# Performance work log

Measured on AMD Instinct MI355X. Metric: run time of the kernel, lower is better.

Reference implementation:

```python
import jax, jax.numpy as jnp
import numpy as np

DIM = 1024
HEADS = 16
HEAD_DIM = DIM // HEADS
SCALE = HEAD_DIM ** -0.5


def setup_inputs() -> dict:
    key = jax.random.key(0)
    k_x, k_win, k_wout, k_bout = jax.random.split(key, 4)
    x = jax.random.normal(k_x, (4, 2048, DIM), dtype=jnp.float32)
    # torch Linear: y = x @ W.T + b; store weights as [in, out] for jnp
    w_in = jax.random.normal(k_win, (DIM, 3 * DIM), dtype=jnp.float32) * (DIM ** -0.5)
    w_out = jax.random.normal(k_wout, (DIM, DIM), dtype=jnp.float32) * (DIM ** -0.5)
    b_out = jax.random.normal(k_bout, (DIM,), dtype=jnp.float32) * 0.02
    return {"x": x, "w_in": w_in, "w_out": w_out, "b_out": b_out}


def reference(x, w_in, w_out, b_out):
    b, n, _ = x.shape
    qkv = x @ w_in  # [b, n, 3*dim]
    q, k, v = jnp.split(qkv, 3, axis=-1)
    # [b, n, h*d] -> [b, h, n, d]
    def split_heads(t):
        return t.reshape(b, n, HEADS, HEAD_DIM).transpose(0, 2, 1, 3)
    q, k, v = split_heads(q), split_heads(k), split_heads(v)
    scores = jnp.einsum('bhid,bhjd->bhij', q, k) * SCALE
    attn = jax.nn.softmax(scores, axis=-1)  # dropout_rate=0 -> identity
    o = jnp.einsum('bhij,bhjd->bhid', attn, v)
    o = o.transpose(0, 2, 1, 3).reshape(b, n, HEADS * HEAD_DIM)
    return o @ w_out + b_out
```

## Files before the change

### kernel.cpp

```cpp
#include <hip/hip_runtime.h>

typedef unsigned short u16;
typedef __bf16 bf16x8 __attribute__((ext_vector_type(8)));
typedef float f32x4 __attribute__((ext_vector_type(4)));
typedef unsigned short u16x4 __attribute__((ext_vector_type(4)));
typedef unsigned short u16x8 __attribute__((ext_vector_type(8)));

#define DIM 1024
#define HEADS 16
#define HD 64
#define SEQ 2048
#define BATCH 4
#define NROWS (BATCH*SEQ)
#define ATT_SCALE 0.125f

__device__ __forceinline__ u16 f2bf(float f) {
  union { float f; unsigned u; } v; v.f = f;
  unsigned r = v.u + 0x7FFFu + ((v.u >> 16) & 1u);
  return (u16)(r >> 16);
}

__device__ __forceinline__ f32x4 mfma16(bf16x8 a, bf16x8 b, f32x4 c) {
  return __builtin_amdgcn_mfma_f32_16x16x32_bf16(a, b, c, 0, 0, 0);
}

__device__ __forceinline__ void gl_lds16(const void* g, void* l) {
  __builtin_amdgcn_global_load_lds(
      (const __attribute__((address_space(1))) void*)g,
      (__attribute__((address_space(3))) void*)l, 16, 0, 0);
}

__global__ __launch_bounds__(256) void cast_f32_bf16(const float* __restrict__ in,
                                                     u16* __restrict__ out) {
  int i = blockIdx.x * 256 + threadIdx.x;
  float4 v = ((const float4*)in)[i];
  u16x4 o = { f2bf(v.x), f2bf(v.y), f2bf(v.z), f2bf(v.w) };
  *(u16x4*)(out + (size_t)i * 4) = o;
}

__global__ __launch_bounds__(256) void transpose_cast(const float* __restrict__ in,
                                                      u16* __restrict__ out,
                                                      int R, int C) {
  __shared__ u16 tile[64][65];
  int c0 = blockIdx.x * 64, r0 = blockIdx.y * 64;
  int tid = threadIdx.x;
#pragma unroll
  for (int i = 0; i < 16; ++i) {
    int idx = tid + i * 256;
    int r = idx >> 6, c = idx & 63;
    tile[c][r] = f2bf(in[(size_t)(r0 + r) * C + c0 + c]);
  }
  __syncthreads();
#pragma unroll
  for (int i = 0; i < 16; ++i) {
    int idx = tid + i * 256;
    int r = idx >> 6, c = idx & 63;
    out[(size_t)(c0 + r) * R + r0 + c] = tile[r][c];
  }
}

__global__ __launch_bounds__(256) void transpose_v(const u16* __restrict__ qkv,
                                                   u16* __restrict__ vT) {
  __shared__ unsigned t32[64][37];
  const int t = blockIdx.x, bh = blockIdx.y;
  const int b = bh >> 4, h = bh & 15;
  const u16* src = qkv + ((size_t)(b * SEQ + t * 64)) * 3072 + 2048 + h * 64;
  const int tid = threadIdx.x;
#pragma unroll
  for (int i = 0; i < 8; ++i) {
    int lin = tid + i * 256;
    int r2 = lin >> 6, c = lin & 63;
    unsigned lo = src[(size_t)(2 * r2) * 3072 + c];
    unsigned hi = src[(size_t)(2 * r2 + 1) * 3072 + c];
    t32[c][r2] = lo | (hi << 16);
  }
  __syncthreads();
  unsigned* dst = (unsigned*)(vT + (size_t)bh * 64 * 2048);
#pragma unroll
  for (int i = 0; i < 8; ++i) {
    int lin = tid + i * 256;
    int d = lin >> 5, r2 = lin & 31;
    dst[(size_t)d * 1024 + t * 32 + r2] = t32[d][r2];
  }
}

template<int OUT_F32>
__global__ __launch_bounds__(256) void gemm_bt(const u16* __restrict__ A,
                                               const u16* __restrict__ BT,
                                               void* __restrict__ Cout,
                                               const float* __restrict__ bias,
                                               int M, int N, int K) {
  __shared__ __align__(16) u16 As[128 * 64];
  __shared__ __align__(16) u16 Bs[128 * 64];
  const int tid = threadIdx.x;
  const int l = tid & 63, w = tid >> 6, g = l >> 4, ln = l & 15;
  const int m0 = blockIdx.y * 128, n0 = blockIdx.x * 128;
  const int wr = w >> 1, wc = w & 1;
  f32x4 acc[4][4];
#pragma unroll
  for (int i = 0; i < 4; ++i)
#pragma unroll
    for (int j = 0; j < 4; ++j) acc[i][j] = (f32x4){0.f, 0.f, 0.f, 0.f};

  const int srow = tid >> 3;
  const int scol = (tid & 7) * 8;
  const u16* Asrc = A  + (size_t)(m0 + srow) * K + scol;
  const u16* Bsrc = BT + (size_t)(n0 + srow) * K + scol;
  char* AsB = (char*)As + (size_t)w * 1024;
  char* BsB = (char*)Bs + (size_t)w * 1024;

  const int nk = K >> 6;
  for (int kt = 0; kt < nk; ++kt) {
    const u16* a0 = Asrc + kt * 64;
    const u16* b0 = Bsrc + kt * 64;
#pragma unroll
    for (int is = 0; is < 4; ++is) {
      gl_lds16(a0 + (size_t)is * 32 * K, AsB + is * 4096);
      gl_lds16(b0 + (size_t)is * 32 * K, BsB + is * 4096);
    }
    __syncthreads();
#pragma unroll
    for (int kk = 0; kk < 2; ++kk) {
      bf16x8 af[4], bfr[4];
#pragma unroll
      for (int i = 0; i < 4; ++i) {
        af[i]  = *(const bf16x8*)(As + (wr * 64 + i * 16 + ln) * 64 + kk * 32 + g * 8);
        bfr[i] = *(const bf16x8*)(Bs + (wc * 64 + i * 16 + ln) * 64 + kk * 32 + g * 8);
      }
#pragma unroll
      for (int mi = 0; mi < 4; ++mi)
#pragma unroll
        for (int ni = 0; ni < 4; ++ni)
          acc[mi][ni] = mfma16(af[mi], bfr[ni], acc[mi][ni]);
    }
    __syncthreads();
  }
#pragma unroll
  for (int mi = 0; mi < 4; ++mi) {
#pragma unroll
    for (int ni = 0; ni < 4; ++ni) {
      int col = n0 + wc * 64 + ni * 16 + ln;
#pragma unroll
      for (int j = 0; j < 4; ++j) {
        int row = m0 + wr * 64 + mi * 16 + g * 4 + j;
        float v = acc[mi][ni][j];
        if (OUT_F32) {
          ((float*)Cout)[(size_t)row * N + col] = v + bias[col];
        } else {
          ((u16*)Cout)[(size_t)row * N + col] = f2bf(v);
        }
      }
    }
  }
}

__global__ __launch_bounds__(256) void attn_kernel(const u16* __restrict__ qkv,
                                                   const u16* __restrict__ vT,
                                                   u16* __restrict__ obuf) {
  __shared__ __align__(16) u16 k_lds[64 * 64];
  __shared__ __align__(16) u16 v_lds[64 * 64];
  const int qt = blockIdx.x, h = blockIdx.y, b = blockIdx.z;
  const int tid = threadIdx.x;
  const int w = tid >> 6, l = tid & 63, g = l >> 4, ln = l & 15;
  const int qrow = qt * 64 + w * 16 + ln;
  const size_t rs = 3 * DIM;
  const u16* qb = qkv + (size_t)(b * SEQ + qrow) * rs + h * HD;
  bf16x8 qf0 = *(const bf16x8*)(qb + g * 8);
  bf16x8 qf1 = *(const bf16x8*)(qb + 32 + g * 8);

  const int krow = tid >> 3;
  const int ksrccol = ((((tid & 7) << 4) ^ ((krow & 7) << 4))) >> 1;
  const u16* kbase = qkv + (size_t)b * SEQ * rs + DIM + h * HD;
  const u16* vtb = vT + (size_t)(b * HEADS + h) * 64 * 2048;
  char* kdst = (char*)k_lds + (size_t)w * 1024;
  char* vdst = (char*)v_lds + (size_t)w * 1024;

  const int swz = (ln & 7) << 4;

  float m = -1e30f, lsum = 0.f;
  f32x4 of[4];
#pragma unroll
  for (int i = 0; i < 4; ++i) of[i] = (f32x4){0.f, 0.f, 0.f, 0.f};

  for (int kv0 = 0; kv0 < SEQ; kv0 += 64) {
    const u16* ks0 = kbase + (size_t)(kv0 + krow) * rs + ksrccol;
    const u16* vs0 = vtb + (size_t)krow * 2048 + kv0 + ksrccol;
    gl_lds16(ks0, kdst);
    gl_lds16(ks0 + (size_t)32 * rs, kdst + 4096);
    gl_lds16(vs0, vdst);
    gl_lds16(vs0 + (size_t)32 * 2048, vdst + 4096);
    __syncthreads();

    f32x4 sacc[4];
#pragma unroll
    for (int f = 0; f < 4; ++f) sacc[f] = (f32x4){0.f, 0.f, 0.f, 0.f};
#pragma unroll
    for (int f = 0; f < 4; ++f) {
      const char* kr = (const char*)k_lds + (f * 16 + ln) * 128;
      bf16x8 a0 = *(const bf16x8*)(kr + ((g * 16) ^ swz));
      bf16x8 a1 = *(const bf16x8*)(kr + ((64 | (g * 16)) ^ swz));
      sacc[f] = mfma16(a0, qf0, sacc[f]);
      sacc[f] = mfma16(a1, qf1, sacc[f]);
    }

    float tm = -1e30f;
#pragma unroll
    for (int f = 0; f < 4; ++f)
#pragma unroll
      for (int j = 0; j < 4; ++j) {
        float s = sacc[f][j] * ATT_SCALE;
        sacc[f][j] = s;
        tm = fmaxf(tm, s);
      }
    tm = fmaxf(tm, __shfl_xor(tm, 16));
    tm = fmaxf(tm, __shfl_xor(tm, 32));
    float mn = fmaxf(m, tm);
    float resc = __expf(m - mn);
    float ps = 0.f;
    union pu { u16x8 u; bf16x8 b; } pf[2];
#pragma unroll
    for (int f = 0; f < 4; ++f)
#pragma unroll
      for (int j = 0; j < 4; ++j) {
        float p = __expf(sacc[f][j] - mn);
        ps += p;
        pf[f >> 1].u[(f & 1) * 4 + j] = f2bf(p);
      }
    ps += __shfl_xor(ps, 16);
    ps += __shfl_xor(ps, 32);
    lsum = lsum * resc + ps;
    m = mn;
#pragma unroll
    for (int fd = 0; fd < 4; ++fd) of[fd] *= resc;

#pragma unroll
    for (int kk = 0; kk < 2; ++kk) {
#pragma unroll
      for (int fd = 0; fd < 4; ++fd) {
        const char* vr = (const char*)v_lds + (fd * 16 + ln) * 128;
        u16x4 lo = *(const u16x4*)(vr + ((64 * kk + 8 * g) ^ swz));
        u16x4 hi = *(const u16x4*)(vr + ((64 * kk + 32 + 8 * g) ^ swz));
        union { u16x8 u; bf16x8 b; } fa;
        fa.u = (u16x8){ lo[0], lo[1], lo[2], lo[3], hi[0], hi[1], hi[2], hi[3] };
        of[fd] = mfma16(fa.b, pf[kk].b, of[fd]);
      }
    }
    __syncthreads();
  }

  float linv = 1.f / lsum;
  u16* orow = obuf + (size_t)(b * SEQ + qrow) * DIM + h * HD;
#pragma unroll
  for (int fd = 0; fd < 4; ++fd) {
    u16x4 ov = { f2bf(of[fd][0] * linv), f2bf(of[fd][1] * linv),
                 f2bf(of[fd][2] * linv), f2bf(of[fd][3] * linv) };
    *(u16x4*)(orow + fd * 16 + g * 4) = ov;
  }
}

extern "C" void kernel_launch(void* const* d_in, const int* in_sizes, int n_in,
                              void* d_out, int out_size, void* d_ws, size_t ws_size,
                              hipStream_t stream) {
  const float* x     = (const float*)d_in[0];
  const float* w_in  = (const float*)d_in[1];
  const float* w_out = (const float*)d_in[2];
  const float* b_out = (const float*)d_in[3];
  float* out = (float*)d_out;

  char* ws = (char*)d_ws;
  u16* xb     = (u16*)(ws);
  u16* vT     = (u16*)(ws);
  u16* w_inT  = (u16*)(ws + (size_t)16 * 1024 * 1024);
  u16* w_outT = (u16*)(ws + (size_t)22 * 1024 * 1024);
  u16* qkv    = (u16*)(ws + (size_t)24 * 1024 * 1024);
  u16* obuf   = (u16*)(ws + (size_t)72 * 1024 * 1024);

  cast_f32_bf16<<<8192, 256, 0, stream>>>(x, xb);
  transpose_cast<<<dim3(48, 16), 256, 0, stream>>>(w_in, w_inT, 1024, 3072);
  transpose_cast<<<dim3(16, 16), 256, 0, stream>>>(w_out, w_outT, 1024, 1024);
  gemm_bt<0><<<dim3(24, 64), 256, 0, stream>>>(xb, w_inT, qkv, nullptr, NROWS, 3 * DIM, DIM);
  transpose_v<<<dim3(32, 64), 256, 0, stream>>>(qkv, vT);
  attn_kernel<<<dim3(32, HEADS, BATCH), 256, 0, stream>>>(qkv, vT, obuf);
  gemm_bt<1><<<dim3(8, 64), 256, 0, stream>>>(obuf, w_outT, out, b_out, NROWS, DIM, DIM);
}
```

Before: 277.3 us.

## Streamline attention softmax with exp2, deferred rescale, packed bf16 converts, XCD-aware grid

New measurement: 255.3 us. 1.09x faster.

```diff
diff --git a/kernel.cpp b/kernel.cpp
--- a/kernel.cpp
+++ b/kernel.cpp
@@ -12,12 +12,19 @@
 #define SEQ 2048
 #define BATCH 4
 #define NROWS (BATCH*SEQ)
-#define ATT_SCALE 0.125f
+#define C2 0.18033688f
+#define DEFER_THR 30.0f
 
 __device__ __forceinline__ u16 f2bf(float f) {
   union { float f; unsigned u; } v; v.f = f;
   unsigned r = v.u + 0x7FFFu + ((v.u >> 16) & 1u);
   return (u16)(r >> 16);
+}
+
+__device__ __forceinline__ unsigned cvt_pk_bf16(float lo, float hi) {
+  unsigned r;
+  asm("v_cvt_pk_bf16_f32 %0, %1, %2" : "=v"(r) : "v"(lo), "v"(hi));
+  return r;
 }
 
 __device__ __forceinline__ f32x4 mfma16(bf16x8 a, bf16x8 b, f32x4 c) {
@@ -159,7 +166,9 @@
                                                    u16* __restrict__ obuf) {
   __shared__ __align__(16) u16 k_lds[64 * 64];
   __shared__ __align__(16) u16 v_lds[64 * 64];
-  const int qt = blockIdx.x, h = blockIdx.y, b = blockIdx.z;
+  const int wg = blockIdx.x;
+  const int j = (wg & 7) * 256 + (wg >> 3);
+  const int qt = j & 31, h = (j >> 5) & 15, b = j >> 9;
   const int tid = threadIdx.x;
   const int w = tid >> 6, l = tid & 63, g = l >> 4, ln = l & 15;
   const int qrow = qt * 64 + w * 16 + ln;
@@ -203,45 +212,46 @@
       sacc[f] = mfma16(a1, qf1, sacc[f]);
     }
 
-    float tm = -1e30f;
+    float tm = -3e38f;
 #pragma unroll
     for (int f = 0; f < 4; ++f)
 #pragma unroll
-      for (int j = 0; j < 4; ++j) {
-        float s = sacc[f][j] * ATT_SCALE;
-        sacc[f][j] = s;
-        tm = fmaxf(tm, s);
-      }
+      for (int jj = 0; jj < 4; ++jj) tm = fmaxf(tm, sacc[f][jj]);
     tm = fmaxf(tm, __shfl_xor(tm, 16));
     tm = fmaxf(tm, __shfl_xor(tm, 32));
-    float mn = fmaxf(m, tm);
-    float resc = __expf(m - mn);
+    if (__any(tm > m + DEFER_THR)) {
+      float mn = fmaxf(m, tm);
+      float rs2 = __builtin_amdgcn_exp2f((m - mn) * C2);
+      lsum *= rs2;
+#pragma unroll
+      for (int fd = 0; fd < 4; ++fd) of[fd] *= rs2;
+      m = mn;
+    }
+    const float mc = m * C2;
     float ps = 0.f;
-    union pu { u16x8 u; bf16x8 b; } pf[2];
-#pragma unroll
-    for (int f = 0; f < 4; ++f)
-#pragma unroll
-      for (int j = 0; j < 4; ++j) {
-        float p = __expf(sacc[f][j] - mn);
-        ps += p;
-        pf[f >> 1].u[(f & 1) * 4 + j] = f2bf(p);
-      }
+    union pu { unsigned wd[4]; bf16x8 b; } pf[2];
+#pragma unroll
+    for (int f = 0; f < 4; ++f) {
+#pragma unroll
+      for (int j2 = 0; j2 < 2; ++j2) {
+        float p0 = __builtin_amdgcn_exp2f(fmaf(sacc[f][2 * j2], C2, -mc));
+        float p1 = __builtin_amdgcn_exp2f(fmaf(sacc[f][2 * j2 + 1], C2, -mc));
+        ps += p0 + p1;
+        pf[f >> 1].wd[(f & 1) * 2 + j2] = cvt_pk_bf16(p0, p1);
+      }
+    }
     ps += __shfl_xor(ps, 16);
     ps += __shfl_xor(ps, 32);
-    lsum = lsum * resc + ps;
-    m = mn;
-#pragma unroll
-    for (int fd = 0; fd < 4; ++fd) of[fd] *= resc;
+    lsum += ps;
 
 #pragma unroll
     for (int kk = 0; kk < 2; ++kk) {
 #pragma unroll
       for (int fd = 0; fd < 4; ++fd) {
         const char* vr = (const char*)v_lds + (fd * 16 + ln) * 128;
-        u16x4 lo = *(const u16x4*)(vr + ((64 * kk + 8 * g) ^ swz));
-        u16x4 hi = *(const u16x4*)(vr + ((64 * kk + 32 + 8 * g) ^ swz));
-        union { u16x8 u; bf16x8 b; } fa;
-        fa.u = (u16x8){ lo[0], lo[1], lo[2], lo[3], hi[0], hi[1], hi[2], hi[3] };
+        union { bf16x8 b; struct { u16x4 lo, hi; } hv; } fa;
+        fa.hv.lo = *(const u16x4*)(vr + ((64 * kk + 8 * g) ^ swz));
+        fa.hv.hi = *(const u16x4*)(vr + ((64 * kk + 32 + 8 * g) ^ swz));
         of[fd] = mfma16(fa.b, pf[kk].b, of[fd]);
       }
     }
@@ -252,9 +262,11 @@
   u16* orow = obuf + (size_t)(b * SEQ + qrow) * DIM + h * HD;
 #pragma unroll
   for (int fd = 0; fd < 4; ++fd) {
-    u16x4 ov = { f2bf(of[fd][0] * linv), f2bf(of[fd][1] * linv),
-                 f2bf(of[fd][2] * linv), f2bf(of[fd][3] * linv) };
-    *(u16x4*)(orow + fd * 16 + g * 4) = ov;
+    unsigned w0 = cvt_pk_bf16(of[fd][0] * linv, of[fd][1] * linv);
+    unsigned w1 = cvt_pk_bf16(of[fd][2] * linv, of[fd][3] * linv);
+    unsigned* dst = (unsigned*)(orow + fd * 16 + g * 4);
+    dst[0] = w0;
+    dst[1] = w1;
   }
 }
 
@@ -280,6 +292,6 @@
   transpose_cast<<<dim3(16, 16), 256, 0, stream>>>(w_out, w_outT, 1024, 1024);
   gemm_bt<0><<<dim3(24, 64), 256, 0, stream>>>(xb, w_inT, qkv, nullptr, NROWS, 3 * DIM, DIM);
   transpose_v<<<dim3(32, 64), 256, 0, stream>>>(qkv, vT);
-  attn_kernel<<<dim3(32, HEADS, BATCH), 256, 0, stream>>>(qkv, vT, obuf);
+  attn_kernel<<<2048, 256, 0, stream>>>(qkv, vT, obuf);
   gemm_bt<1><<<dim3(8, 64), 256, 0, stream>>>(obuf, w_outT, out, b_out, NROWS, DIM, DIM);
 }
```
